# Performance work log

Hardware: AMD Instinct MI355X
Metric: run time of the kernel (lower is better)

Reference implementation:

```python
import jax, jax.numpy as jnp
import numpy as np

N, B, D_IN, HID = 1024, 8, 256, 256
L, SH, LH, GH = 2, 2, 4, 2
H = SH + LH + GH
DH = HID // H
EPS = 1e-5


def _sinusoidal_pe(n, d):
    pos = np.arange(n, dtype=np.float32)[:, None]
    i = np.arange(d, dtype=np.float32)[None, :]
    angle = pos / np.power(10000.0, (2.0 * np.floor(i / 2.0)) / d)
    pe = np.where((np.arange(d) % 2) == 0, np.sin(angle), np.cos(angle))
    return jnp.asarray(pe, jnp.float32)  # (n, d)


def _ln(x, g, b):
    mu = x.mean(-1, keepdims=True)
    var = ((x - mu) ** 2).mean(-1, keepdims=True)
    return (x - mu) * jax.lax.rsqrt(var + EPS) * g + b


def setup_inputs() -> dict:
    key = jax.random.key(0)
    ks = jax.random.split(key, 16)
    s = 0.02
    inp = {
        "nodes": jax.random.normal(ks[0], (N, B, D_IN), jnp.float32),
        "dist": jax.random.randint(ks[1], (B, N, N), 0, 6, jnp.int32),
        "W_in": jax.random.normal(ks[2], (D_IN, HID), jnp.float32) * s,
        "b_in": jnp.zeros((HID,), jnp.float32),
        "ln_in_g": jnp.ones((HID,), jnp.float32),
        "ln_in_b": jnp.zeros((HID,), jnp.float32),
        "Wqkv": jax.random.normal(ks[3], (L, HID, 3 * HID), jnp.float32) * s,
        "bqkv": jnp.zeros((L, 3 * HID), jnp.float32),
        "Wo": jax.random.normal(ks[4], (L, HID, HID), jnp.float32) * s,
        "bo": jnp.zeros((L, HID), jnp.float32),
        "ln1_g": jnp.ones((L, HID), jnp.float32),
        "ln1_b": jnp.zeros((L, HID), jnp.float32),
        "W1": jax.random.normal(ks[5], (L, HID, 2 * HID), jnp.float32) * s,
        "b1": jnp.zeros((L, 2 * HID), jnp.float32),
        "W2": jax.random.normal(ks[6], (L, 2 * HID, HID), jnp.float32) * s,
        "b2": jnp.zeros((L, HID), jnp.float32),
        "ln2_g": jnp.ones((L, HID), jnp.float32),
        "ln2_b": jnp.zeros((L, HID), jnp.float32),
        "bn_g": jnp.ones((HID,), jnp.float32),
        "bn_b": jnp.zeros((HID,), jnp.float32),
    }
    return inp


def reference(nodes, dist, W_in, b_in, ln_in_g, ln_in_b, Wqkv, bqkv, Wo, bo,
              ln1_g, ln1_b, W1, b1, W2, b2, ln2_g, ln2_b, bn_g, bn_b):
    # positional embedding (sinusoidal, added) + dense + LayerNorm; dropout=eval (identity)
    x = nodes + _sinusoidal_pe(N, D_IN)[:, None, :]          # (N,B,D_IN)
    x = _ln(x @ W_in + b_in, ln_in_g, ln_in_b)               # (N,B,HID)

    # dist_to_mask: per-head-group allowed patterns; True in torch mask = disallowed
    short = (dist == 1)[:, None]                             # (B,1,N,N)
    longm = (dist >= 1)[:, None]
    allowed = jnp.concatenate([
        jnp.broadcast_to(short, (B, SH, N, N)),
        jnp.broadcast_to(longm, (B, LH, N, N)),
        jnp.ones((B, GH, N, N), bool),
    ], axis=1)                                               # (B,H,N,N)
    bias = jnp.where(allowed, 0.0, -jnp.inf).astype(x.dtype)

    scale = 1.0 / np.sqrt(DH)
    for l in range(L):
        qkv = x @ Wqkv[l] + bqkv[l]                          # (N,B,3*HID)
        q, k, v = jnp.split(qkv, 3, axis=-1)
        def heads(t):  # (N,B,HID) -> (B,H,N,DH)
            return t.reshape(N, B, H, DH).transpose(1, 2, 0, 3)
        q, k, v = heads(q), heads(k), heads(v)
        s = jnp.einsum('bhnd,bhmd->bhnm', q, k) * scale + bias
        a = jax.nn.softmax(s, axis=-1)
        o = jnp.einsum('bhnm,bhmd->bhnd', a, v)              # (B,H,N,DH)
        o = o.transpose(2, 0, 1, 3).reshape(N, B, HID)
        x = _ln(x + o @ Wo[l] + bo[l], ln1_g[l], ln1_b[l])   # post-norm
        f = jax.nn.relu(x @ W1[l] + b1[l]) @ W2[l] + b2[l]
        x = _ln(x + f, ln2_g[l], ln2_b[l])

    y = x[0]                                                 # (B,HID) first position
    mu = y.mean(0)
    var = ((y - mu) ** 2).mean(0)
    return (y - mu) * jax.lax.rsqrt(var + EPS) * bn_g + bn_b
```

## Files before the change

kernel.cpp:

```cpp
#include <hip/hip_runtime.h>
#include <math.h>

constexpr int Nn = 1024, Bb = 8, HIDc = 256, Hh = 8, DHc = 32;
constexpr int TSTR = 520;

typedef __bf16 bf16x8 __attribute__((ext_vector_type(8)));
typedef __bf16 bf16x4 __attribute__((ext_vector_type(4)));
typedef float  f32x4  __attribute__((ext_vector_type(4)));

struct WCvtArgs {
    const float* src[9];
    int K[9], M[9], dstOff[9], tiles[9];
};

__global__ __launch_bounds__(256)
void prep_k(WCvtArgs a, __bf16* __restrict__ Wt,
            const int* __restrict__ dist, unsigned char* __restrict__ mp,
            const float* __restrict__ nodes, __bf16* __restrict__ xinb)
{
    __shared__ float ts[32][33];
    const int tid = threadIdx.x;
    if (blockIdx.x < 1088) {
        int bid = blockIdx.x, i = 0;
        while (bid >= a.tiles[i]) { bid -= a.tiles[i]; ++i; }
        const int K = a.K[i], M = a.M[i];
        const int tilesM = M >> 5;
        const int m0 = (bid % tilesM) << 5, k0 = (bid / tilesM) << 5;
        const float* src = a.src[i];
        __bf16* dst = Wt + a.dstOff[i];
        const int tx = tid & 31, ty = tid >> 5;
        #pragma unroll
        for (int j = 0; j < 4; ++j)
            ts[ty + 8 * j][tx] = src[(size_t)(k0 + ty + 8 * j) * M + m0 + tx];
        __syncthreads();
        #pragma unroll
        for (int j = 0; j < 4; ++j)
            dst[(size_t)(m0 + ty + 8 * j) * K + k0 + tx] = (__bf16)ts[tx][ty + 8 * j];
    } else if (blockIdx.x < 3136) {
        const int idx = (blockIdx.x - 1088) * 256 + tid;
        const int quad = idx & 3, c = (idx >> 2) & 15, q = (idx >> 6) & 1023, b = idx >> 16;
        const int* dp = dist + ((((size_t)b << 10) + q) << 10) + c * 64 + quad * 4;
        uchar4 out;
        unsigned char* po = &out.x;
        #pragma unroll
        for (int t = 0; t < 4; ++t) {
            const int4 v = *(const int4*)(dp + t * 16);
            unsigned int code = 0;
            const int dd[4] = {v.x, v.y, v.z, v.w};
            #pragma unroll
            for (int r = 0; r < 4; ++r)
                code |= ((dd[r] == 1 ? 1u : 0u) | (dd[r] >= 1 ? 2u : 0u)) << (2 * r);
            po[t] = (unsigned char)code;
        }
        *(uchar4*)(mp + ((((size_t)b << 10) + q) << 8) + (c << 4) + (quad << 2)) = out;
    } else {
        const int idx = (blockIdx.x - 3136) * 256 + tid;
        const int token = idx >> 7, k2 = (idx & 127) * 2;
        const int b = token >> 10, n = token & 1023;
        const float e = (float)k2 * (1.0f / 256.0f);
        const float freq = exp2f(-13.287712379549449f * e);
        const float ang = (float)n * freq;
        const float2 nd = *(const float2*)(nodes + ((size_t)(n * 8 + b)) * 256 + k2);
        __bf16* p = xinb + (size_t)token * 256 + k2;
        p[0] = (__bf16)(nd.x + sinf(ang));
        p[1] = (__bf16)(nd.y + cosf(ang));
    }
}

template<int KK, int NJ>
__device__ __forceinline__ void gemmW(const __bf16* __restrict__ wrow,
                                      const __bf16* __restrict__ x0,
                                      const __bf16* __restrict__ x1,
                                      f32x4 acc[2][2])
{
    constexpr int NKC = KK / 32;
    bf16x8 wA[2][NKC];
    #pragma unroll
    for (int kc = 0; kc < NKC; ++kc)
        #pragma unroll
        for (int t = 0; t < 2; ++t)
            wA[t][kc] = *(const bf16x8*)(wrow + (size_t)(t * 16) * KK + kc * 32);
    #pragma unroll
    for (int t = 0; t < 2; ++t) {
        acc[t][0] = (f32x4){0.f, 0.f, 0.f, 0.f};
        if (NJ == 2) acc[t][1] = (f32x4){0.f, 0.f, 0.f, 0.f};
    }
    #pragma unroll
    for (int kc = 0; kc < NKC; ++kc) {
        const bf16x8 b0 = *(const bf16x8*)(x0 + kc * 32);
        bf16x8 b1;
        if (NJ == 2) b1 = *(const bf16x8*)(x1 + kc * 32);
        #pragma unroll
        for (int t = 0; t < 2; ++t) {
            acc[t][0] = __builtin_amdgcn_mfma_f32_16x16x32_bf16(wA[t][kc], b0, acc[t][0], 0, 0, 0);
            if (NJ == 2)
                acc[t][1] = __builtin_amdgcn_mfma_f32_16x16x32_bf16(wA[t][kc], b1, acc[t][1], 0, 0, 0);
        }
    }
}

template<bool RESID, bool FFN, bool QKV, bool N0ROWS, bool XGATE, bool BNOUT, int NJ>
__global__ __launch_bounds__(512, 2)
void layer_k(const __bf16* __restrict__ Ain, const float* __restrict__ xres,
             const __bf16* __restrict__ w0, const float* __restrict__ b0,
             const float* __restrict__ g1, const float* __restrict__ be1,
             const __bf16* __restrict__ w1, const float* __restrict__ b1_,
             const __bf16* __restrict__ w2, const float* __restrict__ b2_,
             const float* __restrict__ g2, const float* __restrict__ be2,
             const __bf16* __restrict__ wq, const float* __restrict__ bq, int qfull,
             const float* __restrict__ bng, const float* __restrict__ bnb,
             float* __restrict__ xout,
             __bf16* __restrict__ qb, __bf16* __restrict__ kb, __bf16* __restrict__ vtb)
{
    __shared__ __bf16 trans[32][TSTR];
    __shared__ float red[8][32][2];

    const int tid = threadIdx.x;
    const int lane = tid & 63;
    const int wv = tid >> 6;
    const int col = lane & 15, quad = lane >> 4;
    const int row0 = blockIdx.x * (NJ * 16);
    const int ms = wv * 32;

    #pragma unroll
    for (int i = 0; i < NJ; ++i) {
        const int v = i * 512 + tid;
        const int rw = v >> 5, cc = (v & 31) * 8;
        const int rg = N0ROWS ? ((rw & 7) << 10) : (row0 + rw);
        *(bf16x8*)&trans[rw][cc] = *(const bf16x8*)(Ain + (size_t)rg * 256 + cc);
    }
    __syncthreads();

    const __bf16* x0 = &trans[col][quad * 8];
    const __bf16* x1 = &trans[16 + col][quad * 8];
    int tg[2];
    #pragma unroll
    for (int j = 0; j < NJ; ++j)
        tg[j] = N0ROWS ? ((j * 16 + col) & 7) << 10 : (row0 + j * 16 + col);

    f32x4 acc[2][2];
    gemmW<256, NJ>(w0 + (size_t)(ms + col) * 256 + quad * 8, x0, x1, acc);

    float val[2][2][4];
    {
        float4 bb4[2], gm4[2], bt4[2];
        #pragma unroll
        for (int t = 0; t < 2; ++t) {
            const int cb = ms + t * 16 + quad * 4;
            bb4[t] = *(const float4*)&b0[cb];
            gm4[t] = *(const float4*)&g1[cb];
            bt4[t] = *(const float4*)&be1[cb];
        }
        #pragma unroll
        for (int j = 0; j < NJ; ++j) {
            float s1 = 0.f, s2 = 0.f;
            #pragma unroll
            for (int t = 0; t < 2; ++t) {
                float4 xr4 = {0.f, 0.f, 0.f, 0.f};
                if (RESID) xr4 = *(const float4*)&xres[(size_t)tg[j] * 256 + ms + t * 16 + quad * 4];
                const float* bbp = (const float*)&bb4[t];
                const float* xrp = (const float*)&xr4;
                #pragma unroll
                for (int r = 0; r < 4; ++r) {
                    float v = acc[t][j][r] + bbp[r] + xrp[r];
                    val[j][t][r] = v; s1 += v; s2 += v * v;
                }
            }
            s1 += __shfl_xor(s1, 16); s1 += __shfl_xor(s1, 32);
            s2 += __shfl_xor(s2, 16); s2 += __shfl_xor(s2, 32);
            if (quad == 0) { red[wv][j * 16 + col][0] = s1; red[wv][j * 16 + col][1] = s2; }
        }
        __syncthreads();
        #pragma unroll
        for (int j = 0; j < NJ; ++j) {
            const int tk = j * 16 + col;
            float s1 = 0.f, s2 = 0.f;
            #pragma unroll
            for (int w = 0; w < 8; ++w) { s1 += red[w][tk][0]; s2 += red[w][tk][1]; }
            const float mu = s1 * (1.0f / 256.0f);
            const float rv = rsqrtf(s2 * (1.0f / 256.0f) - mu * mu + 1e-5f);
            #pragma unroll
            for (int t = 0; t < 2; ++t) {
                const float* gmp = (const float*)&gm4[t];
                const float* btp = (const float*)&bt4[t];
                bf16x4 o4; float4 of;
                #pragma unroll
                for (int r = 0; r < 4; ++r) {
                    const float o = (val[j][t][r] - mu) * rv * gmp[r] + btp[r];
                    val[j][t][r] = o;
                    o4[r] = (__bf16)o;
                    ((float*)&of)[r] = o;
                }
                *(bf16x4*)&trans[tk][ms + t * 16 + quad * 4] = o4;
                if (!FFN)
                    *(float4*)&xout[(size_t)tg[j] * 256 + ms + t * 16 + quad * 4] = of;
            }
        }
        __syncthreads();
    }

    if (FFN) {
        bf16x4 h1p[2][2][2];
        #pragma unroll
        for (int mh = 0; mh < 2; ++mh) {
            f32x4 a1[2][2];
            gemmW<256, NJ>(w1 + (size_t)(mh * 256 + ms + col) * 256 + quad * 8, x0, x1, a1);
            #pragma unroll
            for (int t = 0; t < 2; ++t) {
                const float4 bh4 = *(const float4*)&b1_[mh * 256 + ms + t * 16 + quad * 4];
                const float* bhp = (const float*)&bh4;
                #pragma unroll
                for (int j = 0; j < NJ; ++j)
                    #pragma unroll
                    for (int r = 0; r < 4; ++r)
                        h1p[mh][j][t][r] = (__bf16)fmaxf(a1[t][j][r] + bhp[r], 0.f);
            }
        }
        __syncthreads();
        #pragma unroll
        for (int mh = 0; mh < 2; ++mh)
            #pragma unroll
            for (int j = 0; j < NJ; ++j)
                #pragma unroll
                for (int t = 0; t < 2; ++t)
                    *(bf16x4*)&trans[j * 16 + col][mh * 256 + ms + t * 16 + quad * 4] = h1p[mh][j][t];
        __syncthreads();

        f32x4 a2[2][2];
        gemmW<512, NJ>(w2 + (size_t)(ms + col) * 512 + quad * 8, x0, x1, a2);

        float4 bb4[2], gm4[2], bt4[2];
        #pragma unroll
        for (int t = 0; t < 2; ++t) {
            const int cb = ms + t * 16 + quad * 4;
            bb4[t] = *(const float4*)&b2_[cb];
            gm4[t] = *(const float4*)&g2[cb];
            bt4[t] = *(const float4*)&be2[cb];
        }
        #pragma unroll
        for (int j = 0; j < NJ; ++j) {
            float s1 = 0.f, s2 = 0.f;
            #pragma unroll
            for (int t = 0; t < 2; ++t) {
                const float* bbp = (const float*)&bb4[t];
                #pragma unroll
                for (int r = 0; r < 4; ++r) {
                    const float v = a2[t][j][r] + bbp[r] + val[j][t][r];
                    val[j][t][r] = v; s1 += v; s2 += v * v;
                }
            }
            s1 += __shfl_xor(s1, 16); s1 += __shfl_xor(s1, 32);
            s2 += __shfl_xor(s2, 16); s2 += __shfl_xor(s2, 32);
            if (quad == 0) { red[wv][j * 16 + col][0] = s1; red[wv][j * 16 + col][1] = s2; }
        }
        __syncthreads();
        #pragma unroll
        for (int j = 0; j < NJ; ++j) {
            const int tk = j * 16 + col;
            float s1 = 0.f, s2 = 0.f;
            #pragma unroll
            for (int w = 0; w < 8; ++w) { s1 += red[w][tk][0]; s2 += red[w][tk][1]; }
            const float mu = s1 * (1.0f / 256.0f);
            const float rv = rsqrtf(s2 * (1.0f / 256.0f) - mu * mu + 1e-5f);
            #pragma unroll
            for (int t = 0; t < 2; ++t) {
                const float* gmp = (const float*)&gm4[t];
                const float* btp = (const float*)&bt4[t];
                bf16x4 o4; float4 of;
                #pragma unroll
                for (int r = 0; r < 4; ++r) {
                    const float o = (val[j][t][r] - mu) * rv * gmp[r] + btp[r];
                    val[j][t][r] = o;
                    o4[r] = (__bf16)o;
                    ((float*)&of)[r] = o;
                }
                if (QKV) *(bf16x4*)&trans[tk][ms + t * 16 + quad * 4] = o4;
                if (!BNOUT) {
                    const bool wr = XGATE ? ((tg[j] & 1023) == 0) : true;
                    if (wr) *(float4*)&xout[(size_t)tg[j] * 256 + ms + t * 16 + quad * 4] = of;
                }
            }
        }
        if (BNOUT) {
            #pragma unroll
            for (int t = 0; t < 2; ++t) {
                const int cb = ms + t * 16 + quad * 4;
                const float4 g4 = *(const float4*)&bng[cb];
                const float4 bB = *(const float4*)&bnb[cb];
                float4 of;
                #pragma unroll
                for (int r = 0; r < 4; ++r) {
                    float s1 = val[0][t][r], s2 = val[0][t][r] * val[0][t][r];
                    s1 += __shfl_xor(s1, 1); s2 += __shfl_xor(s2, 1);
                    s1 += __shfl_xor(s1, 2); s2 += __shfl_xor(s2, 2);
                    s1 += __shfl_xor(s1, 4); s2 += __shfl_xor(s2, 4);
                    s1 += __shfl_xor(s1, 8); s2 += __shfl_xor(s2, 8);
                    const float mu = s1 * (1.0f / 16.0f);
                    const float rv = rsqrtf(s2 * (1.0f / 16.0f) - mu * mu + 1e-5f);
                    ((float*)&of)[r] = (val[0][t][r] - mu) * rv * ((const float*)&g4)[r]
                                       + ((const float*)&bB)[r];
                }
                if (col < 8)
                    *(float4*)&xout[(size_t)col * 256 + cb] = of;
            }
        }
        __syncthreads();
    }

    if (QKV) {
        const int b_ = N0ROWS ? 0 : (row0 >> 10);
        const bool qneed = qfull || ((row0 & 1023) < 128);
        const int h = wv;
        for (int cg = 0; cg < 3; ++cg) {
            if (cg == 0 && !qneed) continue;
            f32x4 aq[2][2];
            gemmW<256, NJ>(wq + (size_t)(cg * 256 + ms + col) * 256 + quad * 8, x0, x1, aq);
            const float qs = (cg == 0) ? 0.25505402616305625f : 1.0f;
            #pragma unroll
            for (int t = 0; t < 2; ++t) {
                const int dhb = t * 16 + quad * 4;
                const float4 bq4 = *(const float4*)&bq[cg * 256 + ms + dhb];
                const float* bqp = (const float*)&bq4;
                #pragma unroll
                for (int j = 0; j < NJ; ++j) {
                    const int n = tg[j] & 1023;
                    if (cg == 2) {
                        #pragma unroll
                        for (int r = 0; r < 4; ++r)
                            vtb[((size_t)(b_ * 8 + h) * 32 + dhb + r) * 1024 + n] =
                                (__bf16)(aq[t][j][r] + bqp[r]);
                    } else {
                        bf16x4 p;
                        #pragma unroll
                        for (int r = 0; r < 4; ++r)
                            p[r] = (__bf16)((aq[t][j][r] + bqp[r]) * qs);
                        __bf16* dst = (cg == 0) ? qb : kb;
                        *(bf16x4*)&dst[((size_t)(b_ * 8 + h) * 1024 + n) * 32 + dhb] = p;
                    }
                }
            }
        }
    }
}

__global__ __launch_bounds__(256)
void attn_mfma(const __bf16* __restrict__ Qb, const __bf16* __restrict__ Kb,
               const __bf16* __restrict__ Vt, const unsigned char* __restrict__ MP,
               __bf16* __restrict__ O)
{
    __shared__ __bf16 pbuf[2][4][2][16][72];
    const int tid = threadIdx.x;
    const int lane = tid & 63;
    const int wv = tid >> 6;
    const int col = lane & 15;
    const int quad = lane >> 4;
    const int xr = blockIdx.x;
    const int bh = ((xr & 7) << 3) | (xr >> 3);
    const int b = bh >> 3, h = bh & 7;
    const int qbase = blockIdx.y * 128 + wv * 32;
    const int hsel = (h < 2) ? 0 : 1;
    const bool masked = (h < 6);

    bf16x8 qf[2];
    #pragma unroll
    for (int j = 0; j < 2; ++j)
        qf[j] = *(const bf16x8*)(Qb + ((size_t)bh * Nn + qbase + j * 16 + col) * DHc + quad * 8);

    bf16x8 onesf;
    {
        const __bf16 one = (__bf16)1.0f, zero = (__bf16)0.0f;
        #pragma unroll
        for (int j = 0; j < 8; ++j) onesf[j] = (col == 0) ? one : zero;
    }

    f32x4 O0[2], O1[2], OL[2];
    #pragma unroll
    for (int j = 0; j < 2; ++j) {
        O0[j] = (f32x4){0.f, 0.f, 0.f, 0.f};
        O1[j] = (f32x4){0.f, 0.f, 0.f, 0.f};
        OL[j] = (f32x4){0.f, 0.f, 0.f, 0.f};
    }
    const f32x4 zf = {0.f, 0.f, 0.f, 0.f};
    const __bf16* kbase = Kb + (size_t)bh * Nn * DHc;

    bf16x8 kf[4];
    #pragma unroll
    for (int t = 0; t < 4; ++t)
        kf[t] = *(const bf16x8*)(kbase + (size_t)(t * 16 + col) * DHc + quad * 8);

    for (int c = 0; c < 16; ++c) {
        bf16x8 kn[4];
        if (c < 15)
            #pragma unroll
            for (int t = 0; t < 4; ++t)
                kn[t] = *(const bf16x8*)(kbase + (size_t)((c + 1) * 64 + t * 16 + col) * DHc + quad * 8);
        uchar4 mk[2];
        if (masked)
            #pragma unroll
            for (int j = 0; j < 2; ++j)
                mk[j] = *(const uchar4*)(MP + ((((size_t)b << 10) + qbase + j * 16 + col) << 8)
                                            + (c << 4) + (quad << 2));
        #pragma unroll
        for (int j = 0; j < 2; ++j) {
            f32x4 S[4];
            #pragma unroll
            for (int t = 0; t < 4; ++t)
                S[t] = __builtin_amdgcn_mfma_f32_16x16x32_bf16(kf[t], qf[j], zf, 0, 0, 0);
            if (masked) {
                const unsigned char mb2[4] = {mk[j].x, mk[j].y, mk[j].z, mk[j].w};
                #pragma unroll
                for (int t = 0; t < 4; ++t)
                    #pragma unroll
                    for (int r = 0; r < 4; ++r)
                        if (!((mb2[t] >> (2 * r + hsel)) & 1)) S[t][r] = -INFINITY;
            }
            #pragma unroll
            for (int t = 0; t < 4; ++t) {
                bf16x4 p4;
                #pragma unroll
                for (int r = 0; r < 4; ++r)
                    p4[r] = (__bf16)__builtin_amdgcn_exp2f(S[t][r]);
                *(bf16x4*)(&pbuf[c & 1][wv][j][col][t * 16 + quad * 4]) = p4;
            }
        }
        const __bf16* vp = Vt + (size_t)bh * DHc * Nn + c * 64 + quad * 8;
        #pragma unroll
        for (int kh = 0; kh < 2; ++kh) {
            const bf16x8 v0 = *(const bf16x8*)(vp + (size_t)col * Nn + kh * 32);
            const bf16x8 v1 = *(const bf16x8*)(vp + (size_t)(col + 16) * Nn + kh * 32);
            #pragma unroll
            for (int j = 0; j < 2; ++j) {
                const bf16x8 pf = *(const bf16x8*)(&pbuf[c & 1][wv][j][col][kh * 32 + quad * 8]);
                O0[j] = __builtin_amdgcn_mfma_f32_16x16x32_bf16(pf, v0, O0[j], 0, 0, 0);
                O1[j] = __builtin_amdgcn_mfma_f32_16x16x32_bf16(pf, v1, O1[j], 0, 0, 0);
                OL[j] = __builtin_amdgcn_mfma_f32_16x16x32_bf16(pf, onesf, OL[j], 0, 0, 0);
            }
        }
        if (c < 15)
            #pragma unroll
            for (int t = 0; t < 4; ++t) kf[t] = kn[t];
    }
    #pragma unroll
    for (int j = 0; j < 2; ++j)
        #pragma unroll
        for (int r = 0; r < 4; ++r) {
            const float Lr = __shfl(OL[j][r], lane & 48);
            const float inv = 1.0f / Lr;
            const int q = qbase + j * 16 + quad * 4 + r;
            __bf16* op = O + ((size_t)(b * 1024 + q)) * 256 + h * 32 + col;
            op[0]  = (__bf16)(O0[j][r] * inv);
            op[16] = (__bf16)(O1[j][r] * inv);
        }
}

extern "C" void kernel_launch(void* const* d_in, const int* in_sizes, int n_in,
                              void* d_out, int out_size, void* d_ws, size_t ws_size,
                              hipStream_t stream)
{
    const float* nodes   = (const float*)d_in[0];
    const int*   dist    = (const int*)  d_in[1];
    const float* W_in    = (const float*)d_in[2];
    const float* b_in    = (const float*)d_in[3];
    const float* ln_in_g = (const float*)d_in[4];
    const float* ln_in_b = (const float*)d_in[5];
    const float* Wqkv    = (const float*)d_in[6];
    const float* bqkv    = (const float*)d_in[7];
    const float* Wo      = (const float*)d_in[8];
    const float* bo      = (const float*)d_in[9];
    const float* ln1_g   = (const float*)d_in[10];
    const float* ln1_b   = (const float*)d_in[11];
    const float* W1      = (const float*)d_in[12];
    const float* b1      = (const float*)d_in[13];
    const float* W2      = (const float*)d_in[14];
    const float* b2      = (const float*)d_in[15];
    const float* ln2_g   = (const float*)d_in[16];
    const float* ln2_b   = (const float*)d_in[17];
    const float* bn_g    = (const float*)d_in[18];
    const float* bn_b    = (const float*)d_in[19];

    char* ws = (char*)d_ws;
    float*  x   = (float*)(ws);
    unsigned char* mp = (unsigned char*)(ws + 8388608);
    __bf16* wt  = (__bf16*)(ws + 10485760);
    __bf16* qb  = (__bf16*)(ws + 12845056);
    __bf16* kb  = (__bf16*)(ws + 17039360);
    __bf16* vtb = (__bf16*)(ws + 21233664);
    __bf16* ob  = (__bf16*)(ws + 25427968);
    __bf16* xinb = ob;

    WCvtArgs wa;
    wa.src[0] = W_in;           wa.K[0] = 256; wa.M[0] = 256; wa.dstOff[0] = 0;
    wa.src[1] = Wqkv;           wa.K[1] = 256; wa.M[1] = 768; wa.dstOff[1] = 65536;
    wa.src[2] = Wqkv + 196608;  wa.K[2] = 256; wa.M[2] = 768; wa.dstOff[2] = 262144;
    wa.src[3] = Wo;             wa.K[3] = 256; wa.M[3] = 256; wa.dstOff[3] = 458752;
    wa.src[4] = Wo + 65536;     wa.K[4] = 256; wa.M[4] = 256; wa.dstOff[4] = 524288;
    wa.src[5] = W1;             wa.K[5] = 256; wa.M[5] = 512; wa.dstOff[5] = 589824;
    wa.src[6] = W1 + 131072;    wa.K[6] = 256; wa.M[6] = 512; wa.dstOff[6] = 720896;
    wa.src[7] = W2;             wa.K[7] = 512; wa.M[7] = 256; wa.dstOff[7] = 851968;
    wa.src[8] = W2 + 131072;    wa.K[8] = 512; wa.M[8] = 256; wa.dstOff[8] = 983040;
    for (int i = 0; i < 9; ++i) wa.tiles[i] = (wa.K[i] >> 5) * (wa.M[i] >> 5);

    prep_k<<<7232, 256, 0, stream>>>(wa, wt, dist, mp, nodes, xinb);

    layer_k<false, false, true, false, false, false, 2><<<256, 512, 0, stream>>>(
        xinb, nullptr, wt, b_in, ln_in_g, ln_in_b,
        nullptr, nullptr, nullptr, nullptr, nullptr, nullptr,
        wt + 65536, bqkv, 1, nullptr, nullptr, x, qb, kb, vtb);

    attn_mfma<<<dim3(64, 8), 256, 0, stream>>>(qb, kb, vtb, mp, ob);

    layer_k<true, true, true, false, true, false, 2><<<256, 512, 0, stream>>>(
        ob, x, wt + 458752, bo, ln1_g, ln1_b,
        wt + 589824, b1, wt + 851968, b2, ln2_g, ln2_b,
        wt + 262144, bqkv + 768, 0, nullptr, nullptr, x, qb, kb, vtb);

    attn_mfma<<<dim3(64, 1), 256, 0, stream>>>(qb, kb, vtb, mp, ob);

    layer_k<true, true, false, true, true, true, 1><<<1, 512, 0, stream>>>(
        ob, x, wt + 524288, bo + 256, ln1_g + 256, ln1_b + 256,
        wt + 720896, b1 + 512, wt + 983040, b2 + 256, ln2_g + 256, ln2_b + 256,
        nullptr, nullptr, 0, bn_g, bn_b, (float*)d_out, nullptr, nullptr, nullptr);
}
```

Measured before the change: 258.6 us.

## Add single-query attention kernel for last layer and prefetch V/mask in attention

The last layer only needs query position 0, so the Q projection is now restricted to the row-0 block and a new dedicated attn_q0 kernel computes attention for that single query per (batch, head), replacing a 64-block MFMA launch that processed 32 queries. The main attention loop now double-buffers V fragments and mask bytes alongside K, so the global loads for the next chunk are issued ahead of use. A scheduling barrier is added in the GEMM helper to keep weight loads grouped before the MFMAs. Register pressure rises from the extra prefetch buffers, and the new kernel does scalar dot products with large shuffle reductions.

```diff
diff --git a/kernel.cpp b/kernel.cpp
--- a/kernel.cpp
+++ b/kernel.cpp
@@ -80,6 +80,7 @@
         #pragma unroll
         for (int t = 0; t < 2; ++t)
             wA[t][kc] = *(const bf16x8*)(wrow + (size_t)(t * 16) * KK + kc * 32);
+    __builtin_amdgcn_sched_barrier(0);
     #pragma unroll
     for (int t = 0; t < 2; ++t) {
         acc[t][0] = (f32x4){0.f, 0.f, 0.f, 0.f};
@@ -309,7 +310,7 @@
 
     if (QKV) {
         const int b_ = N0ROWS ? 0 : (row0 >> 10);
-        const bool qneed = qfull || ((row0 & 1023) < 128);
+        const bool qneed = qfull || ((row0 & 1023) == 0);
         const int h = wv;
         for (int cg = 0; cg < 3; ++cg) {
             if (cg == 0 && !qneed) continue;
@@ -382,24 +383,42 @@
     }
     const f32x4 zf = {0.f, 0.f, 0.f, 0.f};
     const __bf16* kbase = Kb + (size_t)bh * Nn * DHc;
-
-    bf16x8 kf[4];
+    const __bf16* vbase = Vt + (size_t)bh * DHc * Nn;
+    const unsigned char* mbase = MP + ((size_t)b << 18);
+
+    bf16x8 kf[4], vf[4];
+    uchar4 mk[2];
     #pragma unroll
     for (int t = 0; t < 4; ++t)
         kf[t] = *(const bf16x8*)(kbase + (size_t)(t * 16 + col) * DHc + quad * 8);
+    #pragma unroll
+    for (int kh = 0; kh < 2; ++kh) {
+        vf[kh * 2 + 0] = *(const bf16x8*)(vbase + (size_t)col * Nn + kh * 32 + quad * 8);
+        vf[kh * 2 + 1] = *(const bf16x8*)(vbase + (size_t)(col + 16) * Nn + kh * 32 + quad * 8);
+    }
+    if (masked)
+        #pragma unroll
+        for (int j = 0; j < 2; ++j)
+            mk[j] = *(const uchar4*)(mbase + (((size_t)(qbase + j * 16 + col)) << 8) + (quad << 2));
 
     for (int c = 0; c < 16; ++c) {
-        bf16x8 kn[4];
-        if (c < 15)
+        bf16x8 kn[4], vn[4];
+        uchar4 mkn[2];
+        if (c < 15) {
             #pragma unroll
             for (int t = 0; t < 4; ++t)
                 kn[t] = *(const bf16x8*)(kbase + (size_t)((c + 1) * 64 + t * 16 + col) * DHc + quad * 8);
-        uchar4 mk[2];
-        if (masked)
-            #pragma unroll
-            for (int j = 0; j < 2; ++j)
-                mk[j] = *(const uchar4*)(MP + ((((size_t)b << 10) + qbase + j * 16 + col) << 8)
-                                            + (c << 4) + (quad << 2));
+            #pragma unroll
+            for (int kh = 0; kh < 2; ++kh) {
+                vn[kh * 2 + 0] = *(const bf16x8*)(vbase + (size_t)col * Nn + (c + 1) * 64 + kh * 32 + quad * 8);
+                vn[kh * 2 + 1] = *(const bf16x8*)(vbase + (size_t)(col + 16) * Nn + (c + 1) * 64 + kh * 32 + quad * 8);
+            }
+            if (masked)
+                #pragma unroll
+                for (int j = 0; j < 2; ++j)
+                    mkn[j] = *(const uchar4*)(mbase + (((size_t)(qbase + j * 16 + col)) << 8)
+                                                    + ((c + 1) << 4) + (quad << 2));
+        }
         #pragma unroll
         for (int j = 0; j < 2; ++j) {
             f32x4 S[4];
@@ -423,22 +442,21 @@
                 *(bf16x4*)(&pbuf[c & 1][wv][j][col][t * 16 + quad * 4]) = p4;
             }
         }
-        const __bf16* vp = Vt + (size_t)bh * DHc * Nn + c * 64 + quad * 8;
         #pragma unroll
         for (int kh = 0; kh < 2; ++kh) {
-            const bf16x8 v0 = *(const bf16x8*)(vp + (size_t)col * Nn + kh * 32);
-            const bf16x8 v1 = *(const bf16x8*)(vp + (size_t)(col + 16) * Nn + kh * 32);
             #pragma unroll
             for (int j = 0; j < 2; ++j) {
                 const bf16x8 pf = *(const bf16x8*)(&pbuf[c & 1][wv][j][col][kh * 32 + quad * 8]);
-                O0[j] = __builtin_amdgcn_mfma_f32_16x16x32_bf16(pf, v0, O0[j], 0, 0, 0);
-                O1[j] = __builtin_amdgcn_mfma_f32_16x16x32_bf16(pf, v1, O1[j], 0, 0, 0);
+                O0[j] = __builtin_amdgcn_mfma_f32_16x16x32_bf16(pf, vf[kh * 2 + 0], O0[j], 0, 0, 0);
+                O1[j] = __builtin_amdgcn_mfma_f32_16x16x32_bf16(pf, vf[kh * 2 + 1], O1[j], 0, 0, 0);
                 OL[j] = __builtin_amdgcn_mfma_f32_16x16x32_bf16(pf, onesf, OL[j], 0, 0, 0);
             }
         }
-        if (c < 15)
-            #pragma unroll
-            for (int t = 0; t < 4; ++t) kf[t] = kn[t];
+        if (c < 15) {
+            #pragma unroll
+            for (int t = 0; t < 4; ++t) { kf[t] = kn[t]; vf[t] = vn[t]; }
+            mk[0] = mkn[0]; mk[1] = mkn[1];
+        }
     }
     #pragma unroll
     for (int j = 0; j < 2; ++j)
@@ -451,6 +469,73 @@
             op[0]  = (__bf16)(O0[j][r] * inv);
             op[16] = (__bf16)(O1[j][r] * inv);
         }
+}
+
+__global__ __launch_bounds__(256)
+void attn_q0(const __bf16* __restrict__ Qb, const __bf16* __restrict__ Kb,
+             const __bf16* __restrict__ Vt, const unsigned char* __restrict__ MP,
+             __bf16* __restrict__ O)
+{
+    __shared__ float qs[32];
+    __shared__ float osum[4][33];
+    const int tid = threadIdx.x;
+    const int lane = tid & 63, wv = tid >> 6;
+    const int bh = blockIdx.x;
+    const int b = bh >> 3, h = bh & 7;
+    const int hsel = (h < 2) ? 0 : 1;
+    const bool masked = (h < 6);
+
+    if (tid < 32) qs[tid] = (float)Qb[(size_t)bh * 1024 * 32 + tid];
+    __syncthreads();
+    float qr[32];
+    #pragma unroll
+    for (int d = 0; d < 32; ++d) qr[d] = qs[d];
+
+    const int k0 = tid * 4;
+    const __bf16* kp = Kb + ((size_t)bh * 1024 + k0) * 32;
+    unsigned int mbyte = 0xFFu;
+    if (masked)
+        mbyte = MP[((size_t)b << 18) + ((k0 >> 6) << 4) + (((k0 >> 2) & 3) << 2) + ((k0 >> 4) & 3)];
+
+    float p[4], ps = 0.f;
+    #pragma unroll
+    for (int r = 0; r < 4; ++r) {
+        float s = 0.f;
+        #pragma unroll
+        for (int c8 = 0; c8 < 4; ++c8) {
+            const bf16x8 kv = *(const bf16x8*)(kp + r * 32 + c8 * 8);
+            #pragma unroll
+            for (int d = 0; d < 8; ++d) s += (float)kv[d] * qr[c8 * 8 + d];
+        }
+        const bool allow = !masked || ((mbyte >> (2 * r + hsel)) & 1);
+        p[r] = allow ? __builtin_amdgcn_exp2f(s) : 0.f;
+        ps += p[r];
+    }
+
+    float acc[32];
+    #pragma unroll
+    for (int d = 0; d < 32; ++d) {
+        const bf16x4 v4 = *(const bf16x4*)(Vt + ((size_t)bh * 32 + d) * 1024 + k0);
+        acc[d] = p[0] * (float)v4[0] + p[1] * (float)v4[1]
+               + p[2] * (float)v4[2] + p[3] * (float)v4[3];
+    }
+    #pragma unroll
+    for (int off = 1; off < 64; off <<= 1) {
+        ps += __shfl_xor(ps, off);
+        #pragma unroll
+        for (int d = 0; d < 32; ++d) acc[d] += __shfl_xor(acc[d], off);
+    }
+    if (lane == 0) {
+        #pragma unroll
+        for (int d = 0; d < 32; ++d) osum[wv][d] = acc[d];
+        osum[wv][32] = ps;
+    }
+    __syncthreads();
+    if (tid < 32) {
+        const float o = osum[0][tid] + osum[1][tid] + osum[2][tid] + osum[3][tid];
+        const float L = osum[0][32] + osum[1][32] + osum[2][32] + osum[3][32];
+        O[((size_t)(b * 1024)) * 256 + h * 32 + tid] = (__bf16)(o / L);
+    }
 }
 
 extern "C" void kernel_launch(void* const* d_in, const int* in_sizes, int n_in,
@@ -514,7 +599,7 @@
         wt + 589824, b1, wt + 851968, b2, ln2_g, ln2_b,
         wt + 262144, bqkv + 768, 0, nullptr, nullptr, x, qb, kb, vtb);
 
-    attn_mfma<<<dim3(64, 1), 256, 0, stream>>>(qb, kb, vtb, mp, ob);
+    attn_q0<<<64, 256, 0, stream>>>(qb, kb, vtb, mp, ob);
 
     layer_k<true, true, false, true, true, true, 1><<<1, 512, 0, stream>>>(
         ob, x, wt + 524288, bo + 256, ln1_g + 256, ln1_b + 256,
```

Measured after the change: 238.5 us. 1.08x faster.
